# Optimization experiments

Measured on AMD Instinct MI355X. Metric: run time of the kernel, lower is better.

## Reference

```python
import jax, jax.numpy as jnp
import numpy as np

N = 100000      # nodes
E = 1600000     # edges
NG = 512        # graphs in batch
FIN = 7         # in_features
HID = 128       # hidden_channels
OUT = 2         # outfeatures


def setup_inputs() -> dict:
    key = jax.random.key(0)
    ks = jax.random.split(key, 16)
    x = jax.random.normal(ks[0], (N, FIN), jnp.float32)
    edge_index = jax.random.randint(ks[1], (2, E), 0, N, dtype=jnp.int64)
    batch = jnp.sort(jax.random.randint(ks[2], (N,), 0, NG, dtype=jnp.int64))

    def lin_w(k, fan_in, fan_out):
        # glorot-ish init, scale irrelevant for correctness baseline
        return jax.random.normal(k, (fan_in, fan_out), jnp.float32) / np.sqrt(fan_in).astype(np.float32)

    W1 = lin_w(ks[3], FIN, HID); b1 = jnp.zeros((HID,), jnp.float32)
    W2 = lin_w(ks[4], HID, HID); b2 = jnp.zeros((HID,), jnp.float32)
    W3 = lin_w(ks[5], HID, HID); b3 = jnp.zeros((HID,), jnp.float32)
    W4 = lin_w(ks[6], HID, HID); b4 = jnp.zeros((HID,), jnp.float32)
    Wlin = lin_w(ks[7], HID, OUT); blin = jnp.zeros((OUT,), jnp.float32)
    return dict(x=x, edge_index=edge_index, batch=batch,
                W1=W1, b1=b1, W2=W2, b2=b2, W3=W3, b3=b3, W4=W4, b4=b4,
                Wlin=Wlin, blin=blin)


def gcn_conv(h, W, b, src, dst, n):
    # PyG GCNConv: h' = D^{-1/2} (A + I) D^{-1/2} (h W) + b
    # src/dst already include self-loops
    h = h @ W
    deg = jax.ops.segment_sum(jnp.ones(src.shape[0], h.dtype), dst, num_segments=n)
    dinv = jnp.where(deg > 0, jax.lax.rsqrt(deg), jnp.zeros_like(deg))
    norm = dinv[src] * dinv[dst]                       # [E+N]
    agg = jax.ops.segment_sum(norm[:, None] * h[src], dst, num_segments=n)
    return agg + b


def reference(x, edge_index, batch, W1, b1, W2, b2, W3, b3, W4, b4, Wlin, blin):
    loop = jnp.arange(N, dtype=edge_index.dtype)
    src = jnp.concatenate([edge_index[0], loop])       # add self-loops
    dst = jnp.concatenate([edge_index[1], loop])

    h = gcn_conv(x, W1, b1, src, dst, N)
    for W, b in ((W2, b2), (W3, b3), (W4, b4)):
        h = jax.nn.relu(h)
        h = gcn_conv(h, W, b, src, dst, N)

    # global mean pool per graph
    sums = jax.ops.segment_sum(h, batch, num_segments=NG)
    cnt = jax.ops.segment_sum(jnp.ones((N,), h.dtype), batch, num_segments=NG)
    pooled = sums / jnp.maximum(cnt, 1.0)[:, None]     # [NG, HID]

    # dropout is identity in eval mode
    return pooled @ Wlin + blin                        # [NG, OUT]
```

## Files before the change

kernel.cpp:

```cpp
#include <hip/hip_runtime.h>
#include <hip/hip_bf16.h>

#define N_NODES 100000
#define E_EDGES 1600000
#define NG 512
#define FIN 7
#define HID 128
#define NBUCK 782
#define NBLK_SC 256
#define CHUNK 6250
#define TLEN (NBUCK * NBLK_SC)
#define NCH 196
#define MMX_GRID 782
#define AGGW_GRID 25000
#define L1_GRID 25000
#define PROJ_GRID 25000
#define AGG2_GRID 6250

typedef __attribute__((ext_vector_type(8))) short bf16x8;
typedef __attribute__((ext_vector_type(4))) float f32x4;

__device__ __forceinline__ float bf_lo(unsigned int u) { return __uint_as_float(u << 16); }
__device__ __forceinline__ float bf_hi(unsigned int u) { return __uint_as_float(u & 0xffff0000u); }
__device__ __forceinline__ unsigned int f2bf_rne(float f) {
    unsigned int x = __float_as_uint(f);
    return (x + 0x7fffu + ((x >> 16) & 1u)) >> 16;
}
__device__ __forceinline__ unsigned int pack_bf2(float lo, float hi) {
    return f2bf_rne(lo) | (f2bf_rne(hi) << 16);
}


__global__ __launch_bounds__(256) void k_hist2(const int* __restrict__ eidx,
                                               int* __restrict__ table,
                                               const float* __restrict__ W4,
                                               const float* __restrict__ b4,
                                               const float* __restrict__ Wlin,
                                               const float* __restrict__ blin,
                                               float* __restrict__ Wc,
                                               float* __restrict__ bc,
                                               const float* __restrict__ W2,
                                               const float* __restrict__ W3,
                                               unsigned short* __restrict__ WT2,
                                               unsigned short* __restrict__ WT3) {
    __shared__ int h[NBUCK];
    int blk = blockIdx.x, t = threadIdx.x;
    if (blk >= NBLK_SC) {
        int r = blk - NBLK_SC;
        if (r == 0) {
            int k = t >> 1, o = t & 1;
            float acc = 0.f;
            for (int j = 0; j < HID; ++j) acc += W4[k * HID + j] * Wlin[j * 2 + o];
            Wc[k * 2 + o] = acc;
            if (k == 0) {
                float b = blin[o];
                for (int j = 0; j < HID; ++j) b += b4[j] * Wlin[j * 2 + o];
                bc[o] = b;
            }
        } else if (r < 65) {
            int idx = (r - 1) * 256 + t;
            int k = idx >> 7, n = idx & 127;
            WT2[n * 128 + k] = (unsigned short)f2bf_rne(W2[idx]);
        } else {
            int idx = (r - 65) * 256 + t;
            int k = idx >> 7, n = idx & 127;
            WT3[n * 128 + k] = (unsigned short)f2bf_rne(W3[idx]);
        }
        return;
    }
    for (int i = t; i < NBUCK; i += 256) h[i] = 0;
    __syncthreads();
    int e0 = blk * CHUNK, e1 = e0 + CHUNK;
    for (int e = e0 + t; e < e1; e += 256)
        atomicAdd(&h[eidx[E_EDGES + e] >> 7], 1);
    __syncthreads();
    for (int i = t; i < NBUCK; i += 256)
        table[i * NBLK_SC + blk] = h[i];
}

__global__ void k_blocksum(const int* __restrict__ table, int* __restrict__ partial) {
    __shared__ int s[256];
    int b = blockIdx.x, t = threadIdx.x;
    int base = b * 1024;
    int sum = 0;
    for (int i = t; i < 1024; i += 256) {
        int idx = base + i;
        sum += (idx < TLEN) ? table[idx] : 0;
    }
    s[t] = sum; __syncthreads();
    for (int st = 128; st > 0; st >>= 1) {
        if (t < st) s[t] += s[t + st];
        __syncthreads();
    }
    if (t == 0) partial[b] = s[0];
}

__global__ void k_scan_blk(int* __restrict__ partial, int* __restrict__ bucketBase,
                           int* __restrict__ rowptr) {
    __shared__ int s[256];
    int t = threadIdx.x;
    int v = (t < NCH) ? partial[t] : 0;
    s[t] = v; __syncthreads();
    for (int st = 1; st < 256; st <<= 1) {
        int a = (t >= st) ? s[t - st] : 0;
        __syncthreads();
        s[t] += a;
        __syncthreads();
    }
    if (t < NCH) partial[t] = s[t] - v;
    if (t == 0) { bucketBase[NBUCK] = E_EDGES; rowptr[N_NODES] = E_EDGES; }
}

__global__ void k_scan_final(int* __restrict__ table, const int* __restrict__ partial,
                             int* __restrict__ bucketBase) {
    __shared__ int s[1024];
    int b = blockIdx.x, t = threadIdx.x;
    int idx = b * 1024 + t;
    int v = (idx < TLEN) ? table[idx] : 0;
    s[t] = v; __syncthreads();
    for (int st = 1; st < 1024; st <<= 1) {
        int add = (t >= st) ? s[t - st] : 0;
        __syncthreads();
        s[t] += add;
        __syncthreads();
    }
    if (idx < TLEN) {
        int ex = partial[b] + s[t] - v;
        table[idx] = ex;
        if ((idx & (NBLK_SC - 1)) == 0) bucketBase[idx / NBLK_SC] = ex;
    }
}

__global__ __launch_bounds__(256) void k_scatter2(const int* __restrict__ eidx,
                                                  const int* __restrict__ table,
                                                  unsigned int* __restrict__ ebuf) {
    __shared__ int loff[NBUCK];
    int blk = blockIdx.x, t = threadIdx.x;
    for (int i = t; i < NBUCK; i += 256) loff[i] = table[i * NBLK_SC + blk];
    __syncthreads();
    int e0 = blk * CHUNK, e1 = e0 + CHUNK;
    for (int e = e0 + t; e < e1; e += 256) {
        int s = eidx[e];
        int d = eidx[E_EDGES + e];
        int p = atomicAdd(&loff[d >> 7], 1);
        ebuf[p] = ((unsigned int)(d & 127) << 17) | (unsigned int)s;
    }
}

__global__ __launch_bounds__(256) void k_bucket(const unsigned int* __restrict__ ebuf,
                                                const int* __restrict__ bucketBase,
                                                int* __restrict__ rowptr,
                                                float* __restrict__ dinv,
                                                int* __restrict__ col,
                                                const float* __restrict__ x,
                                                float* __restrict__ xs) {
    __shared__ int scnt[128], soff[128], scur[128];
    int b = blockIdx.x, t = threadIdx.x;
    int bbase = bucketBase[b], bend = bucketBase[b + 1];
    if (t < 128) { scnt[t] = 0; scur[t] = 0; }
    __syncthreads();
    for (int e = bbase + t; e < bend; e += 256) {
        unsigned int rec = ebuf[e];
        atomicAdd(&scnt[rec >> 17], 1);
    }
    __syncthreads();
    if (t < 128) soff[t] = scnt[t];
    __syncthreads();
    for (int st = 1; st < 128; st <<= 1) {
        int a = (t < 128 && t >= st) ? soff[t - st] : 0;
        __syncthreads();
        if (t < 128) soff[t] += a;
        __syncthreads();
    }
    float dval = 0.f;
    if (t < 128) {
        int ex = soff[t] - scnt[t];
        int node = b * 128 + t;
        if (node < N_NODES) {
            rowptr[node] = bbase + ex;
            dval = rsqrtf((float)(scnt[t] + 1));
            dinv[node] = dval;
        }
        soff[t] = ex;
    }
    __syncthreads();
    for (int e = bbase + t; e < bend; e += 256) {
        unsigned int rec = ebuf[e];
        int dl = rec >> 17;
        int s = rec & 0x1FFFF;
        int p = bbase + soff[dl] + atomicAdd(&scur[dl], 1);
        col[p] = s;
    }
    if (t < 128) {
        int node = b * 128 + t;
        if (node < N_NODES) {
            float4 v0, v1;
            v0.x = dval * x[node * 7 + 0];
            v0.y = dval * x[node * 7 + 1];
            v0.z = dval * x[node * 7 + 2];
            v0.w = dval * x[node * 7 + 3];
            v1.x = dval * x[node * 7 + 4];
            v1.y = dval * x[node * 7 + 5];
            v1.z = dval * x[node * 7 + 6];
            v1.w = 0.f;
            *(float4*)&xs[node * 8] = v0;
            *(float4*)&xs[node * 8 + 4] = v1;
        }
    }
}


__global__ __launch_bounds__(256) void k_l1(const float* __restrict__ xs,
                                            const float* __restrict__ W1,
                                            const float* __restrict__ b1,
                                            const int* __restrict__ rowptr,
                                            const int* __restrict__ col,
                                            const float* __restrict__ dinv,
                                            unsigned int* __restrict__ g1) {
    __shared__ float w1s[FIN * HID];
    __shared__ float b1s[HID];
    int t = threadIdx.x;
    for (int i = t; i < FIN * HID; i += 256) w1s[i] = W1[i];
    if (t < HID) b1s[t] = b1[t];
    __syncthreads();

    int lane = t & 63, wave = t >> 6;
    int g = lane >> 3, r = lane & 7;
    int node = blockIdx.x * 4 + wave;
    float di = dinv[node];
    float acc = (g == 0) ? xs[node * 8 + r] : 0.f;
    int e0 = rowptr[node], e1 = rowptr[node + 1];

    for (int base = e0; base < e1; base += 64) {
        int m = e1 - base; if (m > 64) m = 64;
        int cv = col[base + lane];
        int j = 0;
        for (; j + 8 <= m; j += 8) {
            int s = __shfl(cv, j + g);
            acc += xs[s * 8 + r];
        }
        if (j < m) {
            int jg = j + g;
            int idx = (jg < m) ? jg : j;
            int s = __shfl(cv, idx);
            float u = xs[s * 8 + r];
            if (jg < m) acc += u;
        }
    }
    acc += __shfl_xor(acc, 8);
    acc += __shfl_xor(acc, 16);
    acc += __shfl_xor(acc, 32);
    acc *= di;

    float av[FIN];
    #pragma unroll
    for (int k = 0; k < FIN; ++k) av[k] = __shfl(acc, k);
    float2 bb = *(const float2*)&b1s[2 * lane];
    float acc0 = bb.x, acc1 = bb.y;
    #pragma unroll
    for (int k = 0; k < FIN; ++k) {
        float2 w = *(const float2*)&w1s[k * HID + 2 * lane];
        acc0 += av[k] * w.x;
        acc1 += av[k] * w.y;
    }
    g1[(size_t)node * 64 + lane] = pack_bf2(di * fmaxf(acc0, 0.f), di * fmaxf(acc1, 0.f));
}


__global__ __launch_bounds__(256) void k_aggW(const unsigned int* __restrict__ gIn,
                                              unsigned int* __restrict__ gOut,
                                              const int* __restrict__ rowptr,
                                              const int* __restrict__ colv,
                                              const float* __restrict__ dinv) {
    int wid = (blockIdx.x * blockDim.x + threadIdx.x) >> 6;
    int lane = threadIdx.x & 63;
    if (wid >= N_NODES) return;
    int i = wid;
    float di = dinv[i];
    int e0 = rowptr[i], e1 = rowptr[i + 1];
    int cv = colv[e0 + lane];
    unsigned int v = gIn[(size_t)i * 64 + lane];
    float ax = bf_lo(v), ay = bf_hi(v);

    for (int base = e0; base < e1; base += 64) {
        int m = e1 - base; if (m > 64) m = 64;
        int cvn = cv;
        if (base + 64 < e1) cvn = colv[base + 64 + lane];
        int j = 0;
        for (; j + 7 < m; j += 8) {
            int s0 = __shfl(cv, j),     s1 = __shfl(cv, j + 1);
            int s2 = __shfl(cv, j + 2), s3 = __shfl(cv, j + 3);
            int s4 = __shfl(cv, j + 4), s5 = __shfl(cv, j + 5);
            int s6 = __shfl(cv, j + 6), s7 = __shfl(cv, j + 7);
            unsigned int u0 = gIn[(size_t)s0 * 64 + lane];
            unsigned int u1 = gIn[(size_t)s1 * 64 + lane];
            unsigned int u2 = gIn[(size_t)s2 * 64 + lane];
            unsigned int u3 = gIn[(size_t)s3 * 64 + lane];
            unsigned int u4 = gIn[(size_t)s4 * 64 + lane];
            unsigned int u5 = gIn[(size_t)s5 * 64 + lane];
            unsigned int u6 = gIn[(size_t)s6 * 64 + lane];
            unsigned int u7 = gIn[(size_t)s7 * 64 + lane];
            ax += bf_lo(u0); ay += bf_hi(u0);
            ax += bf_lo(u1); ay += bf_hi(u1);
            ax += bf_lo(u2); ay += bf_hi(u2);
            ax += bf_lo(u3); ay += bf_hi(u3);
            ax += bf_lo(u4); ay += bf_hi(u4);
            ax += bf_lo(u5); ay += bf_hi(u5);
            ax += bf_lo(u6); ay += bf_hi(u6);
            ax += bf_lo(u7); ay += bf_hi(u7);
        }
        for (; j + 3 < m; j += 4) {
            int s0 = __shfl(cv, j),     s1 = __shfl(cv, j + 1);
            int s2 = __shfl(cv, j + 2), s3 = __shfl(cv, j + 3);
            unsigned int u0 = gIn[(size_t)s0 * 64 + lane];
            unsigned int u1 = gIn[(size_t)s1 * 64 + lane];
            unsigned int u2 = gIn[(size_t)s2 * 64 + lane];
            unsigned int u3 = gIn[(size_t)s3 * 64 + lane];
            ax += bf_lo(u0); ay += bf_hi(u0);
            ax += bf_lo(u1); ay += bf_hi(u1);
            ax += bf_lo(u2); ay += bf_hi(u2);
            ax += bf_lo(u3); ay += bf_hi(u3);
        }
        for (; j < m; ++j) {
            int s0 = __shfl(cv, j);
            unsigned int u0 = gIn[(size_t)s0 * 64 + lane];
            ax += bf_lo(u0); ay += bf_hi(u0);
        }
        cv = cvn;
    }
    gOut[(size_t)i * 64 + lane] = pack_bf2(di * ax, di * ay);
}


__global__ __launch_bounds__(256) void k_mmx(const unsigned int* __restrict__ gIn,
                                             const unsigned short* __restrict__ WTg,
                                             const float* __restrict__ bias,
                                             const float* __restrict__ dinv,
                                             unsigned int* __restrict__ outg) {
    __shared__ unsigned short sbuf[128 * 136];
    int t = threadIdx.x;
    for (int i = t * 8; i < 128 * 128; i += 256 * 8) {
        int n = i >> 7, k = i & 127;
        uint4 val = *(const uint4*)(WTg + i);
        *(uint4*)(sbuf + n * 136 + k) = val;
    }

    int lane = t & 63, wave = t >> 6;
    int m = lane & 15, quad = lane >> 4;
    int nodeBase = blockIdx.x * 128 + wave * 32;
    const short* gs = (const short*)gIn;

    float bi[8];
    #pragma unroll
    for (int nt = 0; nt < 8; ++nt) bi[nt] = bias[nt * 16 + m];

    f32x4 acc[2][8];
    #pragma unroll
    for (int gi = 0; gi < 2; ++gi)
        #pragma unroll
        for (int nt = 0; nt < 8; ++nt)
            acc[gi][nt] = (f32x4){0.f, 0.f, 0.f, 0.f};

    __syncthreads();

    #pragma unroll
    for (int kc = 0; kc < 4; ++kc) {
        bf16x8 ah[2];
        #pragma unroll
        for (int gi = 0; gi < 2; ++gi) {
            int node = nodeBase + gi * 16 + m;
            bf16x8 h = {0, 0, 0, 0, 0, 0, 0, 0};
            if (node < N_NODES)
                h = *(const bf16x8*)(gs + (size_t)node * 128 + kc * 32 + quad * 8);
            ah[gi] = h;
        }
        #pragma unroll
        for (int nt = 0; nt < 8; ++nt) {
            bf16x8 b = *(const bf16x8*)(sbuf + (nt * 16 + m) * 136 + kc * 32 + quad * 8);
            #pragma unroll
            for (int gi = 0; gi < 2; ++gi)
                acc[gi][nt] = __builtin_amdgcn_mfma_f32_16x16x32_bf16(ah[gi], b, acc[gi][nt], 0, 0, 0);
        }
    }

    __syncthreads();
    #pragma unroll
    for (int gi = 0; gi < 2; ++gi)
        #pragma unroll
        for (int r = 0; r < 4; ++r) {
            int nl = wave * 32 + gi * 16 + quad * 4 + r;
            int node = blockIdx.x * 128 + nl;
            float di = (node < N_NODES) ? dinv[node] : 0.f;
            #pragma unroll
            for (int nt = 0; nt < 8; ++nt) {
                float vv = acc[gi][nt][r] + bi[nt];
                sbuf[nl * 132 + nt * 16 + m] = (unsigned short)f2bf_rne(di * fmaxf(vv, 0.f));
            }
        }
    __syncthreads();
    for (int i = t; i < 128 * 32; i += 256) {
        int nl = i >> 5, p = i & 31;
        int node = blockIdx.x * 128 + nl;
        if (node < N_NODES) {
            uint2 val = *(const uint2*)(sbuf + nl * 132 + p * 4);
            *(uint2*)&outg[(size_t)node * 64 + p * 2] = val;
        }
    }
}


__global__ __launch_bounds__(256) void k_proj(const unsigned int* __restrict__ gIn,
                                              const float* __restrict__ Wc,
                                              float2* __restrict__ ps) {
    int wid = (blockIdx.x * blockDim.x + threadIdx.x) >> 6;
    int lane = threadIdx.x & 63;
    unsigned int u = gIn[(size_t)wid * 64 + lane];
    float4 w = *(const float4*)&Wc[lane * 4];
    float p0 = bf_lo(u) * w.x + bf_hi(u) * w.z;
    float p1 = bf_lo(u) * w.y + bf_hi(u) * w.w;
    #pragma unroll
    for (int s = 1; s < 64; s <<= 1) {
        p0 += __shfl_xor(p0, s);
        p1 += __shfl_xor(p1, s);
    }
    if (lane == 0) { float2 o; o.x = p0; o.y = p1; ps[wid] = o; }
}


__global__ __launch_bounds__(256) void k_agg2(const float2* __restrict__ ps,
                                              const int* __restrict__ rowptr,
                                              const int* __restrict__ col,
                                              const float* __restrict__ dinv,
                                              float2* __restrict__ out2) {
    int t = threadIdx.x;
    int node = (blockIdx.x * 256 + t) >> 4;
    int r = t & 15;
    int e0 = rowptr[node], e1 = rowptr[node + 1];
    float a0 = 0.f, a1 = 0.f;
    for (int e = e0 + r; e < e1; e += 16) {
        int s = col[e];
        float2 pv = ps[s];
        a0 += pv.x; a1 += pv.y;
    }
    #pragma unroll
    for (int sh = 1; sh < 16; sh <<= 1) {
        a0 += __shfl_xor(a0, sh);
        a1 += __shfl_xor(a1, sh);
    }
    if (r == 0) {
        float2 pn = ps[node];
        float di = dinv[node];
        float2 o;
        o.x = di * (a0 + pn.x);
        o.y = di * (a1 + pn.y);
        out2[node] = o;
    }
}


__global__ __launch_bounds__(256) void k_pool2(const float2* __restrict__ out2,
                                               const int* __restrict__ batch,
                                               const float* __restrict__ bc,
                                               const float* __restrict__ blin,
                                               float* __restrict__ out) {
    int g = (blockIdx.x * blockDim.x + threadIdx.x) >> 6;
    int lane = threadIdx.x & 63;
    if (g >= NG) return;
    int lo = 0, hi = N_NODES;
    while (lo < hi) { int mid = (lo + hi) >> 1; if (batch[mid] < g) lo = mid + 1; else hi = mid; }
    int start = lo;
    hi = N_NODES;
    while (lo < hi) { int mid = (lo + hi) >> 1; if (batch[mid] < g + 1) lo = mid + 1; else hi = mid; }
    int end = lo, cnt = end - start;
    float a0 = 0.f, a1 = 0.f;
    for (int n = start + lane; n < end; n += 64) {
        float2 v = out2[n];
        a0 += v.x; a1 += v.y;
    }
    #pragma unroll
    for (int sh = 1; sh < 64; sh <<= 1) {
        a0 += __shfl_xor(a0, sh);
        a1 += __shfl_xor(a1, sh);
    }
    if (lane == 0) {
        if (cnt > 0) {
            float ic = 1.0f / (float)cnt;
            out[g * 2]     = a0 * ic + bc[0];
            out[g * 2 + 1] = a1 * ic + bc[1];
        } else {
            out[g * 2]     = blin[0];
            out[g * 2 + 1] = blin[1];
        }
    }
}


extern "C" void kernel_launch(void* const* d_in, const int* in_sizes, int n_in,
                              void* d_out, int out_size, void* d_ws, size_t ws_size,
                              hipStream_t stream) {
    const float* x    = (const float*)d_in[0];
    const int*   eidx = (const int*)d_in[1];
    const int*   batch= (const int*)d_in[2];
    const float* W1   = (const float*)d_in[3];
    const float* b1   = (const float*)d_in[4];
    const float* W2   = (const float*)d_in[5];
    const float* b2   = (const float*)d_in[6];
    const float* W3   = (const float*)d_in[7];
    const float* b3   = (const float*)d_in[8];
    const float* W4   = (const float*)d_in[9];
    const float* b4   = (const float*)d_in[10];
    const float* Wlin = (const float*)d_in[11];
    const float* blin = (const float*)d_in[12];
    float* out = (float*)d_out;

    char* ws = (char*)d_ws;
    size_t off = 0;
    auto carve = [&](size_t bytes) { char* p = ws + off; off = (off + bytes + 255) & ~(size_t)255; return p; };
    int*   rowptr    = (int*)carve((size_t)(N_NODES + 1) * 4);
    float* dinv      = (float*)carve((size_t)N_NODES * 4);
    int*   col       = (int*)carve((size_t)E_EDGES * 4);
    unsigned int* ebuf = (unsigned int*)carve((size_t)E_EDGES * 4);
    int*   table     = (int*)carve((size_t)TLEN * 4);
    int*   partial   = (int*)carve((size_t)NCH * 4);
    int*   bucketBase= (int*)carve((size_t)(NBUCK + 1) * 4);
    float* xs        = (float*)carve((size_t)N_NODES * 8 * 4);
    unsigned int* gA = (unsigned int*)carve((size_t)N_NODES * 64 * 4);
    unsigned int* gB = (unsigned int*)carve((size_t)N_NODES * 64 * 4);
    float2* ps       = (float2*)carve((size_t)N_NODES * 8);
    float2* out2     = (float2*)carve((size_t)N_NODES * 8);
    float* Wc        = (float*)carve((size_t)HID * 2 * 4);
    float* bc        = (float*)carve(2 * 4);
    unsigned short* WT2 = (unsigned short*)carve((size_t)HID * HID * 2);
    unsigned short* WT3 = (unsigned short*)carve((size_t)HID * HID * 2);
    (void)ws_size; (void)n_in; (void)in_sizes; (void)out_size;

    const int BLK = 256;

    k_hist2<<<NBLK_SC + 129, BLK, 0, stream>>>(eidx, table, W4, b4, Wlin, blin,
                                               Wc, bc, W2, W3, WT2, WT3);
    k_blocksum<<<NCH, BLK, 0, stream>>>(table, partial);
    k_scan_blk<<<1, 256, 0, stream>>>(partial, bucketBase, rowptr);
    k_scan_final<<<NCH, 1024, 0, stream>>>(table, partial, bucketBase);
    k_scatter2<<<NBLK_SC, BLK, 0, stream>>>(eidx, table, ebuf);
    k_bucket<<<NBUCK, BLK, 0, stream>>>(ebuf, bucketBase, rowptr, dinv, col, x, xs);

    k_l1<<<L1_GRID, BLK, 0, stream>>>(xs, W1, b1, rowptr, col, dinv, gA);

    k_aggW<<<AGGW_GRID, BLK, 0, stream>>>(gA, gB, rowptr, col, dinv);
    k_mmx<<<MMX_GRID, BLK, 0, stream>>>(gB, WT2, b2, dinv, gA);
    k_aggW<<<AGGW_GRID, BLK, 0, stream>>>(gA, gB, rowptr, col, dinv);
    k_mmx<<<MMX_GRID, BLK, 0, stream>>>(gB, WT3, b3, dinv, gA);

    k_proj<<<PROJ_GRID, BLK, 0, stream>>>(gA, Wc, ps);
    k_agg2<<<AGG2_GRID, BLK, 0, stream>>>(ps, rowptr, col, dinv, out2);
    k_pool2<<<(NG * 64 + BLK - 1) / BLK, BLK, 0, stream>>>(out2, batch, bc, blin, out);
}
```

Measured before the change: 377.2 us.

## Fuse final projection into matmul epilogue and merge aggregation with pooling

Folds the single-block partial scan into the final scan kernel so each block recomputes the small prefix. Computes the 128-to-2 projection directly in the last MFMA kernel epilogue from shared memory, avoiding writing and rereading the full bf16 hidden tensor. Merges the last 2-wide aggregation with mean pooling in a per-graph kernel, removing the intermediate buffer and two launches. The per-graph kernel has much lower parallelism (512 blocks) than the previous per-node aggregation.

```diff
diff --git a/kernel.cpp b/kernel.cpp
--- a/kernel.cpp
+++ b/kernel.cpp
@@ -14,8 +14,6 @@
 #define MMX_GRID 782
 #define AGGW_GRID 25000
 #define L1_GRID 25000
-#define PROJ_GRID 25000
-#define AGG2_GRID 6250
 
 typedef __attribute__((ext_vector_type(8))) short bf16x8;
 typedef __attribute__((ext_vector_type(4))) float f32x4;
@@ -95,26 +93,20 @@
     if (t == 0) partial[b] = s[0];
 }
 
-__global__ void k_scan_blk(int* __restrict__ partial, int* __restrict__ bucketBase,
-                           int* __restrict__ rowptr) {
-    __shared__ int s[256];
-    int t = threadIdx.x;
-    int v = (t < NCH) ? partial[t] : 0;
-    s[t] = v; __syncthreads();
+__global__ void k_scan_final(int* __restrict__ table, const int* __restrict__ partial,
+                             int* __restrict__ bucketBase, int* __restrict__ rowptr) {
+    __shared__ int s[1024];
+    __shared__ int cs[256];
+    int b = blockIdx.x, t = threadIdx.x;
+    if (t < 256) cs[t] = (t < NCH) ? partial[t] : 0;
+    __syncthreads();
     for (int st = 1; st < 256; st <<= 1) {
-        int a = (t >= st) ? s[t - st] : 0;
-        __syncthreads();
-        s[t] += a;
-        __syncthreads();
-    }
-    if (t < NCH) partial[t] = s[t] - v;
-    if (t == 0) { bucketBase[NBUCK] = E_EDGES; rowptr[N_NODES] = E_EDGES; }
-}
-
-__global__ void k_scan_final(int* __restrict__ table, const int* __restrict__ partial,
-                             int* __restrict__ bucketBase) {
-    __shared__ int s[1024];
-    int b = blockIdx.x, t = threadIdx.x;
+        int a = (t < 256 && t >= st) ? cs[t - st] : 0;
+        __syncthreads();
+        if (t < 256) cs[t] += a;
+        __syncthreads();
+    }
+    int chunk_ex = cs[b] - partial[b];
     int idx = b * 1024 + t;
     int v = (idx < TLEN) ? table[idx] : 0;
     s[t] = v; __syncthreads();
@@ -125,10 +117,11 @@
         __syncthreads();
     }
     if (idx < TLEN) {
-        int ex = partial[b] + s[t] - v;
+        int ex = chunk_ex + s[t] - v;
         table[idx] = ex;
         if ((idx & (NBLK_SC - 1)) == 0) bucketBase[idx / NBLK_SC] = ex;
     }
+    if (b == 0 && t == 0) { bucketBase[NBUCK] = E_EDGES; rowptr[N_NODES] = E_EDGES; }
 }
 
 __global__ __launch_bounds__(256) void k_scatter2(const int* __restrict__ eidx,
@@ -336,7 +329,9 @@
                                              const unsigned short* __restrict__ WTg,
                                              const float* __restrict__ bias,
                                              const float* __restrict__ dinv,
-                                             unsigned int* __restrict__ outg) {
+                                             unsigned int* __restrict__ outg,
+                                             const float* __restrict__ Wcp,
+                                             float2* __restrict__ ps) {
     __shared__ unsigned short sbuf[128 * 136];
     int t = threadIdx.x;
     for (int i = t * 8; i < 128 * 128; i += 256 * 8) {
@@ -384,6 +379,8 @@
     }
 
     __syncthreads();
+    float* wcs = (float*)(sbuf + 128 * 132);
+    if (Wcp != nullptr) wcs[t] = Wcp[t];
     #pragma unroll
     for (int gi = 0; gi < 2; ++gi)
         #pragma unroll
@@ -398,95 +395,84 @@
             }
         }
     __syncthreads();
-    for (int i = t; i < 128 * 32; i += 256) {
-        int nl = i >> 5, p = i & 31;
+    if (Wcp == nullptr) {
+        for (int i = t; i < 128 * 32; i += 256) {
+            int nl = i >> 5, p = i & 31;
+            int node = blockIdx.x * 128 + nl;
+            if (node < N_NODES) {
+                uint2 val = *(const uint2*)(sbuf + nl * 132 + p * 4);
+                *(uint2*)&outg[(size_t)node * 64 + p * 2] = val;
+            }
+        }
+    } else {
+        int nl = t >> 1, half = t & 1;
         int node = blockIdx.x * 128 + nl;
-        if (node < N_NODES) {
-            uint2 val = *(const uint2*)(sbuf + nl * 132 + p * 4);
-            *(uint2*)&outg[(size_t)node * 64 + p * 2] = val;
-        }
-    }
-}
-
-
-__global__ __launch_bounds__(256) void k_proj(const unsigned int* __restrict__ gIn,
-                                              const float* __restrict__ Wc,
-                                              float2* __restrict__ ps) {
-    int wid = (blockIdx.x * blockDim.x + threadIdx.x) >> 6;
-    int lane = threadIdx.x & 63;
-    unsigned int u = gIn[(size_t)wid * 64 + lane];
-    float4 w = *(const float4*)&Wc[lane * 4];
-    float p0 = bf_lo(u) * w.x + bf_hi(u) * w.z;
-    float p1 = bf_lo(u) * w.y + bf_hi(u) * w.w;
-    #pragma unroll
-    for (int s = 1; s < 64; s <<= 1) {
-        p0 += __shfl_xor(p0, s);
-        p1 += __shfl_xor(p1, s);
-    }
-    if (lane == 0) { float2 o; o.x = p0; o.y = p1; ps[wid] = o; }
-}
-
-
-__global__ __launch_bounds__(256) void k_agg2(const float2* __restrict__ ps,
+        const unsigned int* row = (const unsigned int*)(sbuf + nl * 132 + half * 64);
+        float p0 = 0.f, p1 = 0.f;
+        #pragma unroll
+        for (int q = 0; q < 32; ++q) {
+            unsigned int u = row[q];
+            float4 w = *(const float4*)&wcs[(half * 64 + 2 * q) * 2];
+            p0 += bf_lo(u) * w.x + bf_hi(u) * w.z;
+            p1 += bf_lo(u) * w.y + bf_hi(u) * w.w;
+        }
+        p0 += __shfl_xor(p0, 1);
+        p1 += __shfl_xor(p1, 1);
+        if (half == 0 && node < N_NODES) { float2 o; o.x = p0; o.y = p1; ps[node] = o; }
+    }
+}
+
+
+__global__ __launch_bounds__(256) void k_tail(const float2* __restrict__ ps,
                                               const int* __restrict__ rowptr,
                                               const int* __restrict__ col,
                                               const float* __restrict__ dinv,
-                                              float2* __restrict__ out2) {
-    int t = threadIdx.x;
-    int node = (blockIdx.x * 256 + t) >> 4;
-    int r = t & 15;
-    int e0 = rowptr[node], e1 = rowptr[node + 1];
-    float a0 = 0.f, a1 = 0.f;
-    for (int e = e0 + r; e < e1; e += 16) {
-        int s = col[e];
-        float2 pv = ps[s];
-        a0 += pv.x; a1 += pv.y;
-    }
-    #pragma unroll
-    for (int sh = 1; sh < 16; sh <<= 1) {
-        a0 += __shfl_xor(a0, sh);
-        a1 += __shfl_xor(a1, sh);
-    }
-    if (r == 0) {
-        float2 pn = ps[node];
-        float di = dinv[node];
-        float2 o;
-        o.x = di * (a0 + pn.x);
-        o.y = di * (a1 + pn.y);
-        out2[node] = o;
-    }
-}
-
-
-__global__ __launch_bounds__(256) void k_pool2(const float2* __restrict__ out2,
-                                               const int* __restrict__ batch,
-                                               const float* __restrict__ bc,
-                                               const float* __restrict__ blin,
-                                               float* __restrict__ out) {
-    int g = (blockIdx.x * blockDim.x + threadIdx.x) >> 6;
-    int lane = threadIdx.x & 63;
-    if (g >= NG) return;
+                                              const int* __restrict__ batch,
+                                              const float* __restrict__ bc,
+                                              const float* __restrict__ blin,
+                                              float* __restrict__ out) {
+    __shared__ float red[8];
+    int g = blockIdx.x, t = threadIdx.x;
     int lo = 0, hi = N_NODES;
     while (lo < hi) { int mid = (lo + hi) >> 1; if (batch[mid] < g) lo = mid + 1; else hi = mid; }
     int start = lo;
     hi = N_NODES;
     while (lo < hi) { int mid = (lo + hi) >> 1; if (batch[mid] < g + 1) lo = mid + 1; else hi = mid; }
     int end = lo, cnt = end - start;
-    float a0 = 0.f, a1 = 0.f;
-    for (int n = start + lane; n < end; n += 64) {
-        float2 v = out2[n];
-        a0 += v.x; a1 += v.y;
-    }
-    #pragma unroll
-    for (int sh = 1; sh < 64; sh <<= 1) {
-        a0 += __shfl_xor(a0, sh);
-        a1 += __shfl_xor(a1, sh);
-    }
-    if (lane == 0) {
+
+    int grp = t >> 4, r = t & 15;
+    float s0 = 0.f, s1 = 0.f;
+    for (int n = start + grp; n < end; n += 16) {
+        int e0 = rowptr[n], e1 = rowptr[n + 1];
+        float a0 = 0.f, a1 = 0.f;
+        for (int e = e0 + r; e < e1; e += 16) {
+            float2 pv = ps[col[e]];
+            a0 += pv.x; a1 += pv.y;
+        }
+        #pragma unroll
+        for (int sh = 1; sh < 16; sh <<= 1) {
+            a0 += __shfl_xor(a0, sh);
+            a1 += __shfl_xor(a1, sh);
+        }
+        if (r == 0) {
+            float2 pn = ps[n];
+            float di = dinv[n];
+            s0 += di * (a0 + pn.x);
+            s1 += di * (a1 + pn.y);
+        }
+    }
+    s0 += __shfl_xor(s0, 16); s1 += __shfl_xor(s1, 16);
+    s0 += __shfl_xor(s0, 32); s1 += __shfl_xor(s1, 32);
+    int lane = t & 63, wave = t >> 6;
+    if (lane == 0) { red[wave * 2] = s0; red[wave * 2 + 1] = s1; }
+    __syncthreads();
+    if (t == 0) {
+        float r0 = red[0] + red[2] + red[4] + red[6];
+        float r1 = red[1] + red[3] + red[5] + red[7];
         if (cnt > 0) {
             float ic = 1.0f / (float)cnt;
-            out[g * 2]     = a0 * ic + bc[0];
-            out[g * 2 + 1] = a1 * ic + bc[1];
+            out[g * 2]     = r0 * ic + bc[0];
+            out[g * 2 + 1] = r1 * ic + bc[1];
         } else {
             out[g * 2]     = blin[0];
             out[g * 2 + 1] = blin[1];
@@ -527,7 +513,6 @@
     unsigned int* gA = (unsigned int*)carve((size_t)N_NODES * 64 * 4);
     unsigned int* gB = (unsigned int*)carve((size_t)N_NODES * 64 * 4);
     float2* ps       = (float2*)carve((size_t)N_NODES * 8);
-    float2* out2     = (float2*)carve((size_t)N_NODES * 8);
     float* Wc        = (float*)carve((size_t)HID * 2 * 4);
     float* bc        = (float*)carve(2 * 4);
     unsigned short* WT2 = (unsigned short*)carve((size_t)HID * HID * 2);
@@ -539,19 +524,16 @@
     k_hist2<<<NBLK_SC + 129, BLK, 0, stream>>>(eidx, table, W4, b4, Wlin, blin,
                                                Wc, bc, W2, W3, WT2, WT3);
     k_blocksum<<<NCH, BLK, 0, stream>>>(table, partial);
-    k_scan_blk<<<1, 256, 0, stream>>>(partial, bucketBase, rowptr);
-    k_scan_final<<<NCH, 1024, 0, stream>>>(table, partial, bucketBase);
+    k_scan_final<<<NCH, 1024, 0, stream>>>(table, partial, bucketBase, rowptr);
     k_scatter2<<<NBLK_SC, BLK, 0, stream>>>(eidx, table, ebuf);
     k_bucket<<<NBUCK, BLK, 0, stream>>>(ebuf, bucketBase, rowptr, dinv, col, x, xs);
 
     k_l1<<<L1_GRID, BLK, 0, stream>>>(xs, W1, b1, rowptr, col, dinv, gA);
 
     k_aggW<<<AGGW_GRID, BLK, 0, stream>>>(gA, gB, rowptr, col, dinv);
-    k_mmx<<<MMX_GRID, BLK, 0, stream>>>(gB, WT2, b2, dinv, gA);
+    k_mmx<<<MMX_GRID, BLK, 0, stream>>>(gB, WT2, b2, dinv, gA, nullptr, nullptr);
     k_aggW<<<AGGW_GRID, BLK, 0, stream>>>(gA, gB, rowptr, col, dinv);
-    k_mmx<<<MMX_GRID, BLK, 0, stream>>>(gB, WT3, b3, dinv, gA);
-
-    k_proj<<<PROJ_GRID, BLK, 0, stream>>>(gA, Wc, ps);
-    k_agg2<<<AGG2_GRID, BLK, 0, stream>>>(ps, rowptr, col, dinv, out2);
-    k_pool2<<<(NG * 64 + BLK - 1) / BLK, BLK, 0, stream>>>(out2, batch, bc, blin, out);
-}
+    k_mmx<<<MMX_GRID, BLK, 0, stream>>>(gB, WT3, b3, dinv, gA, Wc, ps);
+
+    k_tail<<<NG, BLK, 0, stream>>>(ps, rowptr, col, dinv, batch, bc, blin, out);
+}
```

Result: faster. 360.7 us (-4.4%).
